# Kernel optimization log

Hardware: AMD Instinct MI355X
Metric: run time of the kernel (lower is better)

## Reference

```python
import jax, jax.numpy as jnp
import numpy as np

B, L, H, P = 4, 4096, 1024, 256


def _bin_op(ei, ej):
    A_i, Bu_i = ei
    A_j, Bu_j = ej
    return (A_j * A_i, A_j * Bu_i + Bu_j)


def _s5(x, log_real, imag, B_real, B_imag, C_real, C_imag, D, log_Delta):
    Lam = jax.lax.complex(-jnp.exp(log_real), imag)                 # [P]
    B_tilde = jax.lax.complex(B_real, B_imag)                        # [P,H]
    C_tilde = jax.lax.complex(C_real, C_imag)                        # [H,P]
    Delta = jnp.exp(log_Delta)                                       # [P]
    Lambda_bar = jnp.exp(Lam * Delta)                                # [P]
    Lam_safe = jnp.where(jnp.abs(Lam) < 1e-6,
                         jnp.full_like(Lam, 1e-6), Lam)
    B_bar = ((Lambda_bar - 1.0) / Lam_safe)[:, None] * B_tilde       # [P,H]
    Bu = x.astype(jnp.complex64) @ B_bar.T                           # [B,L,P]
    La = jnp.broadcast_to(Lambda_bar[None, None, :], Bu.shape)
    _, xs = jax.lax.associative_scan(_bin_op, (La, Bu), axis=1)      # [B,L,P]
    ys = jnp.real(xs @ C_tilde.T) + D * x                            # [B,L,H]
    return jax.nn.gelu(ys, approximate=False)


def setup_inputs() -> dict:
    key = jax.random.key(0)
    ks = jax.random.split(key, 17)
    std_b = 1.0 / H ** 0.5
    std_c = 1.0 / P ** 0.5
    d = {"x": jax.random.normal(ks[0], (B, L, H), dtype=jnp.float32)}
    for i, pfx in enumerate(["fwd", "bwd"]):
        o = 1 + 8 * i
        d[pfx + "_log_real"] = jax.random.normal(ks[o], (P,)) * 0.5
        d[pfx + "_imag"] = jax.random.normal(ks[o + 1], (P,))
        d[pfx + "_B_real"] = jax.random.normal(ks[o + 2], (P, H)) * std_b
        d[pfx + "_B_imag"] = jax.random.normal(ks[o + 3], (P, H)) * std_b
        d[pfx + "_C_real"] = jax.random.normal(ks[o + 4], (H, P)) * std_c
        d[pfx + "_C_imag"] = jax.random.normal(ks[o + 5], (H, P)) * std_c
        d[pfx + "_D"] = jnp.ones((H,), dtype=jnp.float32)
        d[pfx + "_log_Delta"] = jnp.zeros((P,), dtype=jnp.float32)
    return d


def reference(x,
              fwd_log_real, fwd_imag, fwd_B_real, fwd_B_imag,
              fwd_C_real, fwd_C_imag, fwd_D, fwd_log_Delta,
              bwd_log_real, bwd_imag, bwd_B_real, bwd_B_imag,
              bwd_C_real, bwd_C_imag, bwd_D, bwd_log_Delta):
    y_f = _s5(x, fwd_log_real, fwd_imag, fwd_B_real, fwd_B_imag,
              fwd_C_real, fwd_C_imag, fwd_D, fwd_log_Delta)
    x_flip = jnp.flip(x, axis=1)
    y_b = _s5(x_flip, bwd_log_real, bwd_imag, bwd_B_real, bwd_B_imag,
              bwd_C_real, bwd_C_imag, bwd_D, bwd_log_Delta)
    return y_f + jnp.flip(y_b, axis=1)
```

## Files before the change

kernel.cpp:

```cpp
#include <hip/hip_runtime.h>
#include <math.h>


typedef short bf16x8 __attribute__((ext_vector_type(8)));
typedef float f32x4 __attribute__((ext_vector_type(4)));
typedef unsigned short u16x8 __attribute__((ext_vector_type(8)));

__device__ __forceinline__ unsigned short f2bf(float f) {
  union { float f; unsigned int u; } v; v.f = f;
  unsigned int r = (v.u + 0x7FFFu + ((v.u >> 16) & 1u)) >> 16;
  return (unsigned short)r;
}
__device__ __forceinline__ float bf2f(unsigned short s) {
  union { unsigned int u; float f; } v; v.u = ((unsigned int)s) << 16;
  return v.f;
}
__device__ __forceinline__ float gelu_fast(float v) {
  const float u = 1.5957691216057308f * fmaf(0.044715f * v, v * v, v);
  return v / (1.f + __expf(-u));
}
__device__ __forceinline__ void gload16(const unsigned short* g, void* l) {
  __builtin_amdgcn_global_load_lds(
      (const __attribute__((address_space(1))) void*)g,
      (__attribute__((address_space(3))) void*)l, 16, 0, 0);
}

__global__ __launch_bounds__(256) void cast_prep_kernel(
    const float* __restrict__ x, unsigned short* __restrict__ xbf,
    const float* __restrict__ flr, const float* __restrict__ fim,
    const float* __restrict__ fBr, const float* __restrict__ fBi,
    const float* __restrict__ fCr, const float* __restrict__ fCi,
    const float* __restrict__ flD,
    const float* __restrict__ blr, const float* __restrict__ bim,
    const float* __restrict__ bBr, const float* __restrict__ bBi,
    const float* __restrict__ bCr, const float* __restrict__ bCi,
    const float* __restrict__ blD,
    unsigned short* __restrict__ W, unsigned short* __restrict__ CmT,
    float4* __restrict__ lamp) {
  const int tid = threadIdx.x;
  if (blockIdx.x < 8192) {
    const size_t i = (size_t)blockIdx.x * 256 + tid;
    const float4* xv = (const float4*)x;
    float4 a = xv[2 * i], b = xv[2 * i + 1];
    u16x8 r;
    r[0] = f2bf(a.x); r[1] = f2bf(a.y); r[2] = f2bf(a.z); r[3] = f2bf(a.w);
    r[4] = f2bf(b.x); r[5] = f2bf(b.y); r[6] = f2bf(b.z); r[7] = f2bf(b.w);
    *(u16x8*)(xbf + 8 * i) = r;
    return;
  }
  const int bid = blockIdx.x - 8192;
  if (bid < 512) {
    const int dir = bid >> 8, p = bid & 255;
    const float* lr_ = dir ? blr : flr;
    const float* im_ = dir ? bim : fim;
    const float* lD_ = dir ? blD : flD;
    const float* Br_ = dir ? bBr : fBr;
    const float* Bi_ = dir ? bBi : fBi;
    const float Lre = -expf(lr_[p]);
    const float Lim = im_[p];
    const float Dl = expf(lD_[p]);
    const float ar = Lre * Dl, ai = Lim * Dl;
    const float er = expf(ar);
    const float lre = er * cosf(ai), lim = er * sinf(ai);
    const float e64 = expf(64.f * ar);
    const float l64re = e64 * cosf(64.f * ai), l64im = e64 * sinf(64.f * ai);
    float sre = Lre, sim = Lim;
    if (sqrtf(Lre * Lre + Lim * Lim) < 1e-6f) { sre = 1e-6f; sim = 0.f; }
    const float den = sre * sre + sim * sim;
    const float fre = ((lre - 1.f) * sre + lim * sim) / den;
    const float fi2 = (lim * sre - (lre - 1.f) * sim) / den;
    if (tid == 0) lamp[dir * 256 + p] = make_float4(lre, lim, l64re, l64im);
    const size_t rowR = (size_t)(dir * 512 + 2 * p) * 1024;
    const size_t rowI = rowR + 1024;
    for (int h = tid; h < 1024; h += 256) {
      const float Br = Br_[p * 1024 + h], Bi = Bi_[p * 1024 + h];
      W[rowR + h] = f2bf(fre * Br - fi2 * Bi);
      W[rowI + h] = f2bf(fre * Bi + fi2 * Br);
    }
  } else {
    const int h = bid - 512;
    for (int k = tid; k < 1024; k += 256) {
      const int dir = k >> 9, within = k & 511;
      const int p = within >> 1, comp = within & 1;
      const float* C = comp ? (dir ? bCi : fCi) : (dir ? bCr : fCr);
      float v = C[(size_t)h * 256 + p];
      if (comp) v = -v;
      CmT[(size_t)h * 1024 + k] = f2bf(v);
    }
  }
}

#define GEMM_STAGE(BUF, KT, APTR, BPTR)                                        \
  {                                                                            \
    const int k0 = (KT) << 6;                                                  \
    _Pragma("unroll") for (int i = 0; i < 4; ++i) {                            \
      const int r = (i << 5) + tr;                                             \
      const int o = ((BUF) << 14) + (i << 12) + (tid << 4);                    \
      gload16(APTR + (size_t)(m0 + r) * 1024 + (k0 + csw), (char*)As + o);     \
      gload16(BPTR + (size_t)(n0 + r) * 1024 + (k0 + csw), (char*)Bs + o);     \
    }                                                                          \
  }

#define GEMM_COMPUTE(BUF, ACC)                                                 \
  {                                                                            \
    const int bo = (BUF) << 13;               \
    _Pragma("unroll") for (int kk = 0; kk < 64; kk += 32) {                    \
      bf16x8 af[4], bf_[4];                                                    \
      _Pragma("unroll") for (int m4 = 0; m4 < 4; ++m4) {                       \
        const int row = (wm << 6) + (m4 << 4) + fr;                            \
        af[m4] = *(const bf16x8*)&As[bo + row * 64 + ((kk + ks) ^ sw)];        \
      }                                                                        \
      _Pragma("unroll") for (int n4 = 0; n4 < 4; ++n4) {                       \
        const int row = (wn << 6) + (n4 << 4) + fr;                            \
        bf_[n4] = *(const bf16x8*)&Bs[bo + row * 64 + ((kk + ks) ^ sw)];       \
      }                                                                        \
      _Pragma("unroll") for (int m4 = 0; m4 < 4; ++m4)                         \
          _Pragma("unroll") for (int n4 = 0; n4 < 4; ++n4)                     \
              ACC[m4][n4] = __builtin_amdgcn_mfma_f32_16x16x32_bf16(           \
                  af[m4], bf_[n4], ACC[m4][n4], 0, 0, 0);                      \
    }                                                                          \
  }

#define PIPE_PUBLISH8()                                                        \
  asm volatile("s_waitcnt vmcnt(8)" ::: "memory");                             \
  __builtin_amdgcn_sched_barrier(0);                                           \
  __builtin_amdgcn_s_barrier();                                                \
  __builtin_amdgcn_sched_barrier(0);

#define PIPE_CLOSE()                                                           \
  __builtin_amdgcn_sched_barrier(0);                                           \
  __builtin_amdgcn_s_barrier();                                                \
  __builtin_amdgcn_sched_barrier(0);

__global__ __launch_bounds__(256) void gemm1_kernel(
    const unsigned short* __restrict__ xbf, const unsigned short* __restrict__ W,
    unsigned short* __restrict__ Zb) {
  __shared__ unsigned short As[2 * 128 * 64];
  __shared__ unsigned short Bs[2 * 128 * 64];
  const int tid = threadIdx.x;
  const int lane = tid & 63;
  const int w = tid >> 6;
  const int wm = w >> 1, wn = w & 1;
  const int fr = lane & 15;
  const int ks = (lane >> 4) << 3;
  const int sw = (fr & 7) << 3;
  const int tr = tid >> 3;
  const int csw = ((tid & 7) ^ (tr & 7)) << 3;
  const int bsw = ((blockIdx.x & 7) << 7) + (blockIdx.x >> 3);
  const int nt = bsw & 7, mt = bsw >> 3;
  const int m0 = mt << 7, n0 = nt << 7;

  f32x4 acc[4][4] = {};

  GEMM_STAGE(0, 0, xbf, W);
  int cur = 0;
  for (int kt = 0; kt < 15; ++kt) {
    GEMM_STAGE(cur ^ 1, kt + 1, xbf, W);
    PIPE_PUBLISH8();
    GEMM_COMPUTE(cur, acc);
    PIPE_CLOSE();
    cur ^= 1;
  }
  __syncthreads();
  GEMM_COMPUTE(cur, acc);

  const int rb = (lane >> 4) << 2;
#pragma unroll
  for (int m4 = 0; m4 < 4; ++m4)
#pragma unroll
    for (int n4 = 0; n4 < 4; ++n4) {
      const size_t gn = n0 + (wn << 6) + (n4 << 4) + fr;
#pragma unroll
      for (int r = 0; r < 4; ++r) {
        const size_t gm = m0 + (wm << 6) + (m4 << 4) + rb + r;
        Zb[gm * 1024 + gn] = f2bf(acc[m4][n4][r]);
      }
    }
}

__global__ __launch_bounds__(256) void scanA_kernel(
    unsigned int* __restrict__ Zp, const float4* __restrict__ lamp,
    float2* __restrict__ part) {
  const int p = threadIdx.x;
  const int k = blockIdx.x & 63;
  const int s = blockIdx.x >> 6;
  const int dir = s & 1, b = s >> 1;
  const float4 lp = lamp[dir * 256 + p];
  const float lre = lp.x, lim = lp.y;
  const size_t col = (size_t)dir * 256 + p;
  const size_t mbase = (size_t)b * 4096 + (size_t)k * 64;
  float sre = 0.f, sim = 0.f;
  if (dir == 0) {
    for (int i = 0; i < 64; ++i) {
      const size_t idx = (mbase + i) * 512 + col;
      const unsigned int u = Zp[idx];
      const float nr = fmaf(lre, sre, fmaf(-lim, sim, bf2f((unsigned short)u)));
      const float ni = fmaf(lre, sim, fmaf(lim, sre, bf2f((unsigned short)(u >> 16))));
      sre = nr; sim = ni;
      Zp[idx] = (unsigned int)f2bf(sre) | ((unsigned int)f2bf(sim) << 16);
    }
  } else {
    for (int i = 63; i >= 0; --i) {
      const size_t idx = (mbase + i) * 512 + col;
      const unsigned int u = Zp[idx];
      const float nr = fmaf(lre, sre, fmaf(-lim, sim, bf2f((unsigned short)u)));
      const float ni = fmaf(lre, sim, fmaf(lim, sre, bf2f((unsigned short)(u >> 16))));
      sre = nr; sim = ni;
      Zp[idx] = (unsigned int)f2bf(sre) | ((unsigned int)f2bf(sim) << 16);
    }
  }
  part[(size_t)(s * 64 + k) * 256 + p] = make_float2(sre, sim);
}

__global__ __launch_bounds__(256) void scanC_kernel(
    const unsigned int* __restrict__ Zp, const float4* __restrict__ lamp,
    const float2* __restrict__ part, unsigned int* __restrict__ xsbf) {
  const int p = threadIdx.x;
  const int k = blockIdx.x & 63;
  const int s = blockIdx.x >> 6;
  const int dir = s & 1, b = s >> 1;
  const float4 lp = lamp[dir * 256 + p];
  const float lre = lp.x, lim = lp.y, wr64 = lp.z, wi64 = lp.w;
  const size_t col = (size_t)dir * 256 + p;
  const size_t mbase = (size_t)b * 4096 + (size_t)k * 64;

  float cr = 0.f, ci = 0.f, wr = 1.f, wi = 0.f;
  if (dir == 0) {
    for (int j = k - 1; j >= 0; --j) {
      const float2 S = part[(size_t)(s * 64 + j) * 256 + p];
      cr = fmaf(wr, S.x, fmaf(-wi, S.y, cr));
      ci = fmaf(wr, S.y, fmaf(wi, S.x, ci));
      const float t = wr * wr64 - wi * wi64;
      wi = wr * wi64 + wi * wr64; wr = t;
    }
  } else {
    for (int j = k + 1; j < 64; ++j) {
      const float2 S = part[(size_t)(s * 64 + j) * 256 + p];
      cr = fmaf(wr, S.x, fmaf(-wi, S.y, cr));
      ci = fmaf(wr, S.y, fmaf(wi, S.x, ci));
      const float t = wr * wr64 - wi * wi64;
      wi = wr * wi64 + wi * wr64; wr = t;
    }
  }

  float qr = lre * cr - lim * ci;
  float qi = lre * ci + lim * cr;
  if (dir == 0) {
    for (int i = 0; i < 64; ++i) {
      const size_t idx = (mbase + i) * 512 + col;
      const unsigned int u = Zp[idx];
      const float vr = bf2f((unsigned short)u) + qr;
      const float vi = bf2f((unsigned short)(u >> 16)) + qi;
      xsbf[idx] = (unsigned int)f2bf(vr) | ((unsigned int)f2bf(vi) << 16);
      const float t = lre * qr - lim * qi;
      qi = lre * qi + lim * qr; qr = t;
    }
  } else {
    for (int i = 63; i >= 0; --i) {
      const size_t idx = (mbase + i) * 512 + col;
      const unsigned int u = Zp[idx];
      const float vr = bf2f((unsigned short)u) + qr;
      const float vi = bf2f((unsigned short)(u >> 16)) + qi;
      xsbf[idx] = (unsigned int)f2bf(vr) | ((unsigned int)f2bf(vi) << 16);
      const float t = lre * qr - lim * qi;
      qi = lre * qi + lim * qr; qr = t;
    }
  }
}

__global__ __launch_bounds__(256, 2) void gemm2_kernel(
    const unsigned short* __restrict__ A2, const unsigned short* __restrict__ CmT,
    const unsigned short* __restrict__ xbf, const float* __restrict__ Df,
    const float* __restrict__ Db, float* __restrict__ out) {
  __shared__ unsigned short As[2 * 128 * 64];
  __shared__ unsigned short Bs[2 * 128 * 64];
  const int tid = threadIdx.x;
  const int lane = tid & 63;
  const int w = tid >> 6;
  const int wm = w >> 1, wn = w & 1;
  const int fr = lane & 15;
  const int ks = (lane >> 4) << 3;
  const int sw = (fr & 7) << 3;
  const int tr = tid >> 3;
  const int csw = ((tid & 7) ^ (tr & 7)) << 3;
  const int bsw = ((blockIdx.x & 7) << 7) + (blockIdx.x >> 3);
  const int nt = bsw & 7, mt = bsw >> 3;
  const int m0 = mt << 7, n0 = nt << 7;

  f32x4 accf[4][4] = {};
  f32x4 accb[4][4] = {};

  GEMM_STAGE(0, 0, A2, CmT);
  int cur = 0;
#pragma unroll
  for (int kt = 0; kt < 8; ++kt) {
    GEMM_STAGE(cur ^ 1, kt + 1, A2, CmT);
    PIPE_PUBLISH8();
    GEMM_COMPUTE(cur, accf);
    PIPE_CLOSE();
    cur ^= 1;
  }
#pragma unroll
  for (int kt = 8; kt < 15; ++kt) {
    GEMM_STAGE(cur ^ 1, kt + 1, A2, CmT);
    PIPE_PUBLISH8();
    GEMM_COMPUTE(cur, accb);
    PIPE_CLOSE();
    cur ^= 1;
  }
  __syncthreads();
  GEMM_COMPUTE(cur, accb);

  const int rb = (lane >> 4) << 2;
#pragma unroll
  for (int n4 = 0; n4 < 4; ++n4) {
    const size_t gn = n0 + (wn << 6) + (n4 << 4) + fr;
    const float dfv = Df[gn], dbv = Db[gn];
#pragma unroll
    for (int m4 = 0; m4 < 4; ++m4) {
#pragma unroll
      for (int r = 0; r < 4; ++r) {
        const size_t gm = m0 + (wm << 6) + (m4 << 4) + rb + r;
        const float xv = bf2f(xbf[gm * 1024 + gn]);
        out[gm * 1024 + gn] = gelu_fast(accf[m4][n4][r] + dfv * xv) +
                              gelu_fast(accb[m4][n4][r] + dbv * xv);
      }
    }
  }
}

extern "C" void kernel_launch(void* const* d_in, const int* in_sizes, int n_in,
                              void* d_out, int out_size, void* d_ws, size_t ws_size,
                              hipStream_t stream) {
  const float* x = (const float*)d_in[0];
  const float* flr = (const float*)d_in[1];
  const float* fim = (const float*)d_in[2];
  const float* fBr = (const float*)d_in[3];
  const float* fBi = (const float*)d_in[4];
  const float* fCr = (const float*)d_in[5];
  const float* fCi = (const float*)d_in[6];
  const float* fD  = (const float*)d_in[7];
  const float* flD = (const float*)d_in[8];
  const float* blr = (const float*)d_in[9];
  const float* bim = (const float*)d_in[10];
  const float* bBr = (const float*)d_in[11];
  const float* bBi = (const float*)d_in[12];
  const float* bCr = (const float*)d_in[13];
  const float* bCi = (const float*)d_in[14];
  const float* bD  = (const float*)d_in[15];
  const float* blD = (const float*)d_in[16];

  char* ws = (char*)d_ws;
  unsigned short* xbf  = (unsigned short*)(ws);
  unsigned short* W    = (unsigned short*)(ws + 33554432);
  unsigned short* CmT  = (unsigned short*)(ws + 35651584);
  unsigned short* Zb   = (unsigned short*)(ws + 37748736);
  unsigned short* xsbf = (unsigned short*)(ws + 71303168);
  float4*         lamp = (float4*)(ws + 104857600);
  float2*         part = (float2*)(ws + 104865792);

  dim3 blk(256);
  cast_prep_kernel<<<9728, blk, 0, stream>>>(
      x, xbf, flr, fim, fBr, fBi, fCr, fCi, flD,
      blr, bim, bBr, bBi, bCr, bCi, blD, W, CmT, lamp);
  gemm1_kernel<<<1024, blk, 0, stream>>>(xbf, W, Zb);
  scanA_kernel<<<512, blk, 0, stream>>>((unsigned int*)Zb, lamp, part);
  scanC_kernel<<<512, blk, 0, stream>>>((unsigned int*)Zb, lamp, part,
                                        (unsigned int*)xsbf);
  gemm2_kernel<<<1024, blk, 0, stream>>>(xsbf, CmT, xbf, fD, bD, (float*)d_out);
}
```

Baseline: 151.2 us.

## Enlarge gemm1 to 256x256 tiles with 512 threads and phased MFMA compute

The first GEMM (x @ B_bar) moves from 128x128 tiles with 256 threads to 256x256 tiles with 512 threads (8 waves, 2x4 layout). Each wave now computes a 128x64 sub-tile, loads its B fragments once per stage, and streams A fragments in four phases, wrapping MFMA bursts in s_setprio. The goal is higher arithmetic intensity and fewer redundant global/LDS loads per FLOP. The cost is 128KB of LDS per block and more accumulator registers, and only 256 blocks, which may underfill the device.

Result: faster. 145.9 us (-3.5%).

```diff
diff --git a/kernel.cpp b/kernel.cpp
--- a/kernel.cpp
+++ b/kernel.cpp
@@ -90,90 +90,94 @@
   }
 }
 
-#define GEMM_STAGE(BUF, KT, APTR, BPTR)                                        \
+#define G1_STAGE(BUF, KT)                                                      \
   {                                                                            \
     const int k0 = (KT) << 6;                                                  \
     _Pragma("unroll") for (int i = 0; i < 4; ++i) {                            \
-      const int r = (i << 5) + tr;                                             \
-      const int o = ((BUF) << 14) + (i << 12) + (tid << 4);                    \
-      gload16(APTR + (size_t)(m0 + r) * 1024 + (k0 + csw), (char*)As + o);     \
-      gload16(BPTR + (size_t)(n0 + r) * 1024 + (k0 + csw), (char*)Bs + o);     \
+      const int r = (i << 6) + tr;                                             \
+      const int o = ((BUF) << 15) + (i << 13) + (tid << 4);                    \
+      gload16(xbf + (size_t)(m0 + r) * 1024 + (k0 + csw), (char*)As + o);      \
+      gload16(W + (size_t)(n0 + r) * 1024 + (k0 + csw), (char*)Bs + o);        \
     }                                                                          \
   }
 
-#define GEMM_COMPUTE(BUF, ACC)                                                 \
+#define G1_COMPUTE(BUF, ACC)                                                   \
   {                                                                            \
-    const int bo = (BUF) << 13;               \
-    _Pragma("unroll") for (int kk = 0; kk < 64; kk += 32) {                    \
-      bf16x8 af[4], bf_[4];                                                    \
-      _Pragma("unroll") for (int m4 = 0; m4 < 4; ++m4) {                       \
-        const int row = (wm << 6) + (m4 << 4) + fr;                            \
-        af[m4] = *(const bf16x8*)&As[bo + row * 64 + ((kk + ks) ^ sw)];        \
+    const int bo = (BUF) << 14;                            \
+    bf16x8 bF[4][2];                                                           \
+    _Pragma("unroll") for (int n4 = 0; n4 < 4; ++n4)                           \
+        _Pragma("unroll") for (int kk2 = 0; kk2 < 2; ++kk2) {                  \
+      const int row = (wn << 6) + (n4 << 4) + fr;                              \
+      bF[n4][kk2] =                                                            \
+          *(const bf16x8*)&Bs[bo + row * 64 + (((kk2 << 5) + ks) ^ sw)];       \
+    }                                                                          \
+    _Pragma("unroll") for (int ph = 0; ph < 4; ++ph) {                         \
+      bf16x8 aF[2][2];                                                         \
+      _Pragma("unroll") for (int mf2 = 0; mf2 < 2; ++mf2)                      \
+          _Pragma("unroll") for (int kk2 = 0; kk2 < 2; ++kk2) {                \
+        const int row = (wm << 7) + (((ph << 1) + mf2) << 4) + fr;             \
+        aF[mf2][kk2] =                                                         \
+            *(const bf16x8*)&As[bo + row * 64 + (((kk2 << 5) + ks) ^ sw)];     \
       }                                                                        \
-      _Pragma("unroll") for (int n4 = 0; n4 < 4; ++n4) {                       \
-        const int row = (wn << 6) + (n4 << 4) + fr;                            \
-        bf_[n4] = *(const bf16x8*)&Bs[bo + row * 64 + ((kk + ks) ^ sw)];       \
-      }                                                                        \
-      _Pragma("unroll") for (int m4 = 0; m4 < 4; ++m4)                         \
+      __builtin_amdgcn_s_setprio(1);                                           \
+      _Pragma("unroll") for (int mf2 = 0; mf2 < 2; ++mf2)                      \
           _Pragma("unroll") for (int n4 = 0; n4 < 4; ++n4)                     \
-              ACC[m4][n4] = __builtin_amdgcn_mfma_f32_16x16x32_bf16(           \
-                  af[m4], bf_[n4], ACC[m4][n4], 0, 0, 0);                      \
+              _Pragma("unroll") for (int kk2 = 0; kk2 < 2; ++kk2)              \
+                  ACC[(ph << 1) + mf2][n4] =                                   \
+                      __builtin_amdgcn_mfma_f32_16x16x32_bf16(                 \
+                          aF[mf2][kk2], bF[n4][kk2], ACC[(ph << 1) + mf2][n4], \
+                          0, 0, 0);                                            \
+      __builtin_amdgcn_s_setprio(0);                                           \
     }                                                                          \
   }
 
-#define PIPE_PUBLISH8()                                                        \
-  asm volatile("s_waitcnt vmcnt(8)" ::: "memory");                             \
-  __builtin_amdgcn_sched_barrier(0);                                           \
-  __builtin_amdgcn_s_barrier();                                                \
-  __builtin_amdgcn_sched_barrier(0);
-
-#define PIPE_CLOSE()                                                           \
-  __builtin_amdgcn_sched_barrier(0);                                           \
-  __builtin_amdgcn_s_barrier();                                                \
-  __builtin_amdgcn_sched_barrier(0);
-
-__global__ __launch_bounds__(256) void gemm1_kernel(
+__global__ __launch_bounds__(512, 2) void gemm1_kernel(
     const unsigned short* __restrict__ xbf, const unsigned short* __restrict__ W,
     unsigned short* __restrict__ Zb) {
-  __shared__ unsigned short As[2 * 128 * 64];
-  __shared__ unsigned short Bs[2 * 128 * 64];
+  __shared__ unsigned short As[2 * 256 * 64];
+  __shared__ unsigned short Bs[2 * 256 * 64];
   const int tid = threadIdx.x;
   const int lane = tid & 63;
   const int w = tid >> 6;
-  const int wm = w >> 1, wn = w & 1;
+  const int wm = w >> 2, wn = w & 3;
   const int fr = lane & 15;
   const int ks = (lane >> 4) << 3;
   const int sw = (fr & 7) << 3;
   const int tr = tid >> 3;
   const int csw = ((tid & 7) ^ (tr & 7)) << 3;
-  const int bsw = ((blockIdx.x & 7) << 7) + (blockIdx.x >> 3);
-  const int nt = bsw & 7, mt = bsw >> 3;
-  const int m0 = mt << 7, n0 = nt << 7;
-
-  f32x4 acc[4][4] = {};
-
-  GEMM_STAGE(0, 0, xbf, W);
+  const int bsw = ((blockIdx.x & 7) << 5) + (blockIdx.x >> 3);
+  const int nt = bsw & 3, mt = bsw >> 2;
+  const int m0 = mt << 8, n0 = nt << 8;
+
+  f32x4 acc[8][4] = {};
+
+  G1_STAGE(0, 0);
   int cur = 0;
   for (int kt = 0; kt < 15; ++kt) {
-    GEMM_STAGE(cur ^ 1, kt + 1, xbf, W);
-    PIPE_PUBLISH8();
-    GEMM_COMPUTE(cur, acc);
-    PIPE_CLOSE();
+    G1_STAGE(cur ^ 1, kt + 1);
+    asm volatile("s_waitcnt vmcnt(8)" ::: "memory");
+    __builtin_amdgcn_sched_barrier(0);
+    __builtin_amdgcn_s_barrier();
+    __builtin_amdgcn_sched_barrier(0);
+    G1_COMPUTE(cur, acc);
+    __builtin_amdgcn_sched_barrier(0);
+    __builtin_amdgcn_s_barrier();
+    __builtin_amdgcn_sched_barrier(0);
     cur ^= 1;
   }
   __syncthreads();
-  GEMM_COMPUTE(cur, acc);
+  G1_COMPUTE(cur, acc);
 
   const int rb = (lane >> 4) << 2;
 #pragma unroll
-  for (int m4 = 0; m4 < 4; ++m4)
+  for (int mf = 0; mf < 8; ++mf)
 #pragma unroll
     for (int n4 = 0; n4 < 4; ++n4) {
       const size_t gn = n0 + (wn << 6) + (n4 << 4) + fr;
 #pragma unroll
       for (int r = 0; r < 4; ++r) {
-        const size_t gm = m0 + (wm << 6) + (m4 << 4) + rb + r;
-        Zb[gm * 1024 + gn] = f2bf(acc[m4][n4][r]);
+        const size_t gm = m0 + (wm << 7) + (mf << 4) + rb + r;
+        Zb[gm * 1024 + gn] = f2bf(acc[mf][n4][r]);
       }
     }
 }
@@ -268,6 +272,48 @@
   }
 }
 
+#define GEMM_STAGE(BUF, KT, APTR, BPTR)                                        \
+  {                                                                            \
+    const int k0 = (KT) << 6;                                                  \
+    _Pragma("unroll") for (int i = 0; i < 4; ++i) {                            \
+      const int r = (i << 5) + tr;                                             \
+      const int o = ((BUF) << 14) + (i << 12) + (tid << 4);                    \
+      gload16(APTR + (size_t)(m0 + r) * 1024 + (k0 + csw), (char*)As + o);     \
+      gload16(BPTR + (size_t)(n0 + r) * 1024 + (k0 + csw), (char*)Bs + o);     \
+    }                                                                          \
+  }
+
+#define GEMM_COMPUTE(BUF, ACC)                                                 \
+  {                                                                            \
+    const int bo = (BUF) << 13;               \
+    _Pragma("unroll") for (int kk = 0; kk < 64; kk += 32) {                    \
+      bf16x8 af[4], bf_[4];                                                    \
+      _Pragma("unroll") for (int m4 = 0; m4 < 4; ++m4) {                       \
+        const int row = (wm << 6) + (m4 << 4) + fr;                            \
+        af[m4] = *(const bf16x8*)&As[bo + row * 64 + ((kk + ks) ^ sw)];        \
+      }                                                                        \
+      _Pragma("unroll") for (int n4 = 0; n4 < 4; ++n4) {                       \
+        const int row = (wn << 6) + (n4 << 4) + fr;                            \
+        bf_[n4] = *(const bf16x8*)&Bs[bo + row * 64 + ((kk + ks) ^ sw)];       \
+      }                                                                        \
+      _Pragma("unroll") for (int m4 = 0; m4 < 4; ++m4)                         \
+          _Pragma("unroll") for (int n4 = 0; n4 < 4; ++n4)                     \
+              ACC[m4][n4] = __builtin_amdgcn_mfma_f32_16x16x32_bf16(           \
+                  af[m4], bf_[n4], ACC[m4][n4], 0, 0, 0);                      \
+    }                                                                          \
+  }
+
+#define PIPE_PUBLISH8()                                                        \
+  asm volatile("s_waitcnt vmcnt(8)" ::: "memory");                             \
+  __builtin_amdgcn_sched_barrier(0);                                           \
+  __builtin_amdgcn_s_barrier();                                                \
+  __builtin_amdgcn_sched_barrier(0);
+
+#define PIPE_CLOSE()                                                           \
+  __builtin_amdgcn_sched_barrier(0);                                           \
+  __builtin_amdgcn_s_barrier();                                                \
+  __builtin_amdgcn_sched_barrier(0);
+
 __global__ __launch_bounds__(256, 2) void gemm2_kernel(
     const unsigned short* __restrict__ A2, const unsigned short* __restrict__ CmT,
     const unsigned short* __restrict__ xbf, const float* __restrict__ Df,
@@ -359,13 +405,12 @@
   float4*         lamp = (float4*)(ws + 104857600);
   float2*         part = (float2*)(ws + 104865792);
 
-  dim3 blk(256);
-  cast_prep_kernel<<<9728, blk, 0, stream>>>(
+  cast_prep_kernel<<<9728, 256, 0, stream>>>(
       x, xbf, flr, fim, fBr, fBi, fCr, fCi, flD,
       blr, bim, bBr, bBi, bCr, bCi, blD, W, CmT, lamp);
-  gemm1_kernel<<<1024, blk, 0, stream>>>(xbf, W, Zb);
-  scanA_kernel<<<512, blk, 0, stream>>>((unsigned int*)Zb, lamp, part);
-  scanC_kernel<<<512, blk, 0, stream>>>((unsigned int*)Zb, lamp, part,
+  gemm1_kernel<<<256, 512, 0, stream>>>(xbf, W, Zb);
+  scanA_kernel<<<512, 256, 0, stream>>>((unsigned int*)Zb, lamp, part);
+  scanC_kernel<<<512, 256, 0, stream>>>((unsigned int*)Zb, lamp, part,
                                         (unsigned int*)xsbf);
-  gemm2_kernel<<<1024, blk, 0, stream>>>(xsbf, CmT, xbf, fD, bD, (float*)d_out);
-}
+  gemm2_kernel<<<1024, 256, 0, stream>>>(xsbf, CmT, xbf, fD, bD, (float*)d_out);
+}
```
